# Optimization experiments

Measured on AMD Instinct MI355X. Metric: run time of the kernel, lower is better.

## Reference

```python
import jax, jax.numpy as jnp
import numpy as np

B, S, D, UNITS = 8, 2048, 1024, 1024

def setup_inputs() -> dict:
    key = jax.random.key(0)
    k1, k2, k3, k4 = jax.random.split(key, 4)
    scale = 1.0 / np.sqrt(D)
    return {
        "inputs": jax.random.normal(k1, (B, S, D), dtype=jnp.float32),
        "Wq": jax.random.normal(k2, (D, UNITS), dtype=jnp.float32) * scale,
        "Wk": jax.random.normal(k3, (D, UNITS), dtype=jnp.float32) * scale,
        "Wv": jax.random.normal(k4, (D, UNITS), dtype=jnp.float32) * scale,
    }

def reference(inputs, Wq, Wk, Wv):
    # QKV projections (bias-free Dense): [B,S,D] @ [D,U] -> [B,S,U]
    q = jnp.einsum("bsd,du->bsu", inputs, Wq)
    k = jnp.einsum("bsd,du->bsu", inputs, Wk)
    v = jnp.einsum("bsd,du->bsu", inputs, Wv)
    # scaled dot-product scores [B,S,S]
    scores = jnp.einsum("bqu,bku->bqk", q, k) / jnp.sqrt(jnp.float32(UNITS))
    attn = jax.nn.softmax(scores, axis=-1)
    # weighted sum of values [B,S,U]
    return jnp.einsum("bqk,bku->bqu", attn, v)
```

## Files before the change

kernel.cpp:

```cpp
#include <hip/hip_runtime.h>


typedef _Float16 half8  __attribute__((ext_vector_type(8)));
typedef _Float16 half4v __attribute__((ext_vector_type(4)));
typedef _Float16 half2v __attribute__((ext_vector_type(2)));
typedef float    floatx4 __attribute__((ext_vector_type(4)));

__device__ __forceinline__ void stage_ht(const _Float16* __restrict__ src, int ld,
                                         _Float16* __restrict__ dst, int wave, int lane) {
#pragma unroll
    for (int i = 0; i < 2; ++i) {
        int q = wave * 2 + i;
        int c = q * 64 + lane;
        int row = c >> 3, c8 = c & 7;
        int cg = c8 ^ (row & 7);
        __builtin_amdgcn_global_load_lds(
            (const __attribute__((address_space(1))) unsigned int*)(src + (size_t)row * ld + cg * 8),
            (__attribute__((address_space(3))) unsigned int*)(dst + q * 512),
            16, 0, 0);
    }
}

__device__ __forceinline__ float sum8h(half8 a) {
    union { half8 v; half2v h2[4]; } u; u.v = a;
    half2v s0 = u.h2[0] + u.h2[1];
    half2v s1 = u.h2[2] + u.h2[3];
    half2v s  = s0 + s1;
    return (float)s[0] + (float)s[1];
}

#define BARF() do { __builtin_amdgcn_s_barrier(); asm volatile("" ::: "memory"); } while (0)

#define SA_(T, h) stage_ht(A + (size_t)((h) * 128) * lda + (size_t)(T) * 64, lda, \
                           ShA + (((T) & 1) * 2 + (h)) * 8192, wave, lane)
#define SB_(T, h) stage_ht(B + (size_t)((h) * 128) * ldb + (size_t)(T) * 64, ldb, \
                           ShB + (((T) & 1) * 2 + (h)) * 8192, wave, lane)

__device__ __forceinline__ void read_b(const _Float16* __restrict__ Bs, int rb,
                                       int l15, int q4, int kk, half8 (&bf)[4]) {
#pragma unroll
    for (int j = 0; j < 4; ++j) {
        int rr = rb + j * 16 + l15;
        int cg = (kk * 4 + q4) ^ (rr & 7);
        bf[j] = *(const half8*)(Bs + rr * 64 + cg * 8);
    }
}

template<bool RSUM>
__device__ __forceinline__ void read_a(const _Float16* __restrict__ As, int i0,
                                       int l15, int q4, int kk, half8 (&af)[4],
                                       float* rsum) {
#pragma unroll
    for (int ii = 0; ii < 4; ++ii) {
        int rr = (i0 + ii) * 16 + l15;
        int cg = (kk * 4 + q4) ^ (rr & 7);
        af[ii] = *(const half8*)(As + rr * 64 + cg * 8);
        if (RSUM) rsum[i0 + ii] += sum8h(af[ii]);
    }
}

__device__ __forceinline__ void mfma16(const half8 (&af)[4], const half8 (&bf)[4],
                                       int i0, floatx4 (&acc)[8][4]) {
    asm volatile("s_waitcnt lgkmcnt(0)" ::: "memory");
    __builtin_amdgcn_sched_barrier(0);
    __builtin_amdgcn_s_setprio(1);
#pragma unroll
    for (int ii = 0; ii < 4; ++ii)
#pragma unroll
        for (int j = 0; j < 4; ++j)
            acc[i0 + ii][j] = __builtin_amdgcn_mfma_f32_16x16x32_f16(
                af[ii], bf[j], acc[i0 + ii][j], 0, 0, 0);
    __builtin_amdgcn_s_setprio(0);
}

template<bool RSUM>
__device__ __forceinline__ void gemm8p(const _Float16* __restrict__ A, int lda,
                                       const _Float16* __restrict__ B, int ldb,
                                       int K, _Float16* __restrict__ ShA,
                                       _Float16* __restrict__ ShB,
                                       int wave, int lane,
                                       floatx4 (&acc)[8][4], float (&rsum)[8]) {
    const int wm = wave >> 2, wn = wave & 3;
    const int l15 = lane & 15, q4 = lane >> 4;
    const int NT = K >> 6;

    SB_(0, 0); SB_(0, 1); SA_(0, 0); SA_(0, 1);
    SB_(1, 0); SB_(1, 1);
    asm volatile("s_waitcnt vmcnt(4)" ::: "memory");
    BARF();

    for (int t = 0; t < NT; ++t) {
        const _Float16* As = ShA + (t & 1) * 16384 + wm * 8192;
        const _Float16* Bs = ShB + (t & 1) * 16384 + (wn >> 1) * 8192;
        const int rb = (wn & 1) * 64;
        half8 bf[4], af[4];

        read_b(Bs, rb, l15, q4, 0, bf);
        read_a<RSUM>(As, 0, l15, q4, 0, af, rsum);
        if (t + 1 < NT) SA_(t + 1, 0);
        BARF();
        mfma16(af, bf, 0, acc);
        BARF();

        read_a<RSUM>(As, 4, l15, q4, 0, af, rsum);
        if (t + 1 < NT) SA_(t + 1, 1);
        BARF();
        mfma16(af, bf, 4, acc);
        BARF();

        read_b(Bs, rb, l15, q4, 1, bf);
        read_a<RSUM>(As, 0, l15, q4, 1, af, rsum);
        BARF();
        mfma16(af, bf, 0, acc);
        BARF();

        read_a<RSUM>(As, 4, l15, q4, 1, af, rsum);
        if (t + 2 < NT) { SB_(t + 2, 0); SB_(t + 2, 1); }
        BARF();
        mfma16(af, bf, 4, acc);
        if (t + 1 < NT) {
            if (t + 2 < NT) asm volatile("s_waitcnt vmcnt(4)" ::: "memory");
            else            asm volatile("s_waitcnt vmcnt(0)" ::: "memory");
        }
        BARF();
    }
}

__global__ void cast_x(const float* __restrict__ X, _Float16* __restrict__ Xh) {
    size_t i = ((size_t)blockIdx.x * 256 + threadIdx.x) * 8;
    float4 v0 = *(const float4*)(X + i);
    float4 v1 = *(const float4*)(X + i + 4);
    half8 hh;
    hh[0] = (_Float16)v0.x; hh[1] = (_Float16)v0.y; hh[2] = (_Float16)v0.z; hh[3] = (_Float16)v0.w;
    hh[4] = (_Float16)v1.x; hh[5] = (_Float16)v1.y; hh[6] = (_Float16)v1.z; hh[7] = (_Float16)v1.w;
    *(half8*)(Xh + i) = hh;
}

__global__ void prep_weights(const float* __restrict__ Wq, const float* __restrict__ Wk,
                             const float* __restrict__ Wv, _Float16* __restrict__ WbT) {
    int g = blockIdx.z;
    const float* W = (g == 0) ? Wq : (g == 1) ? Wk : Wv;
    __shared__ float tile[32][33];
    int u0 = blockIdx.x * 32, d0 = blockIdx.y * 32;
    int tx = threadIdx.x & 31, ty = threadIdx.x >> 5;
#pragma unroll
    for (int i = 0; i < 32; i += 8)
        tile[ty + i][tx] = W[(size_t)(d0 + ty + i) * 1024 + (u0 + tx)];
    __syncthreads();
#pragma unroll
    for (int i = 0; i < 32; i += 8)
        WbT[(size_t)g * 1024 * 1024 + (size_t)(u0 + ty + i) * 1024 + (d0 + tx)] =
            (_Float16)tile[tx][ty + i];
}

__global__ __launch_bounds__(512, 2)
void qkv_gemm(const _Float16* __restrict__ Xh, const _Float16* __restrict__ WbT,
              _Float16* __restrict__ Qh, _Float16* __restrict__ Kh,
              _Float16* __restrict__ Vt) {
    __shared__ __align__(16) _Float16 ShA[32768];
    __shared__ __align__(16) _Float16 ShB[32768];
    int t = threadIdx.x;
    int lane = t & 63, wave = t >> 6;
    int wm = wave >> 2, wn = wave & 3;
    int l15 = lane & 15, q4 = lane >> 4;
    int which = blockIdx.x >> 2;
    int u0 = (blockIdx.x & 3) * 256;
    int m0 = blockIdx.y * 256;
    const _Float16* A = Xh + (size_t)m0 * 1024;
    const _Float16* B = WbT + (size_t)which * 1024 * 1024 + (size_t)u0 * 1024;
    floatx4 acc[8][4] = {};
    float rsum[8] = {};
    gemm8p<false>(A, 1024, B, 1024, 1024, ShA, ShB, wave, lane, acc, rsum);

    int bz = m0 >> 11;
    int sbase = (m0 & 2047) + wm * 128;
    if (which < 2) {
        _Float16* db = (which ? Kh : Qh) + (size_t)bz * 2048 * 1024;
#pragma unroll
        for (int i = 0; i < 8; ++i)
#pragma unroll
            for (int j = 0; j < 4; ++j)
#pragma unroll
                for (int r = 0; r < 4; ++r) {
                    int s = sbase + i * 16 + q4 * 4 + r;
                    int u = u0 + wn * 64 + j * 16 + l15;
                    db[(size_t)s * 1024 + u] = (_Float16)acc[i][j][r];
                }
    } else {
        _Float16* vb = Vt + (size_t)bz * 1024 * 2048;
#pragma unroll
        for (int i = 0; i < 8; ++i)
#pragma unroll
            for (int j = 0; j < 4; ++j) {
                int s = sbase + i * 16 + q4 * 4;
                int u = u0 + wn * 64 + j * 16 + l15;
                half4v pk;
#pragma unroll
                for (int r = 0; r < 4; ++r) pk[r] = (_Float16)acc[i][j][r];
                *(half4v*)(vb + (size_t)u * 2048 + s) = pk;
            }
    }
}

__global__ __launch_bounds__(512, 2)
void scores_gemm(const _Float16* __restrict__ Qh, const _Float16* __restrict__ Kh,
                 _Float16* __restrict__ P) {
    __shared__ __align__(16) _Float16 ShA[32768];
    __shared__ __align__(16) _Float16 ShB[32768];
    int t = threadIdx.x;
    int lane = t & 63, wave = t >> 6;
    int wm = wave >> 2, wn = wave & 3;
    int l15 = lane & 15, q4 = lane >> 4;
    int m0 = blockIdx.y * 256, n0 = blockIdx.x * 256;
    int batch = blockIdx.z;
    const _Float16* A = Qh + (size_t)batch * 2048 * 1024 + (size_t)m0 * 1024;
    const _Float16* B = Kh + (size_t)batch * 2048 * 1024 + (size_t)n0 * 1024;
    floatx4 acc[8][4] = {};
    float rsum[8] = {};
    gemm8p<false>(A, 1024, B, 1024, 1024, ShA, ShB, wave, lane, acc, rsum);

    _Float16* Pb = P + (size_t)batch * 2048 * 2048;
#pragma unroll
    for (int i = 0; i < 8; ++i)
#pragma unroll
        for (int j = 0; j < 4; ++j)
#pragma unroll
            for (int r = 0; r < 4; ++r) {
                int m = m0 + wm * 128 + i * 16 + q4 * 4 + r;
                int n = n0 + wn * 64 + j * 16 + l15;
                Pb[(size_t)m * 2048 + n] = (_Float16)__expf(acc[i][j][r] * 0.03125f);
            }
}

__global__ __launch_bounds__(512, 2)
void pv_gemm(const _Float16* __restrict__ P, const _Float16* __restrict__ Vt,
             float* __restrict__ out) {
    __shared__ __align__(16) _Float16 ShA[32768];
    __shared__ __align__(16) _Float16 ShB[32768];
    int t = threadIdx.x;
    int lane = t & 63, wave = t >> 6;
    int wm = wave >> 2, wn = wave & 3;
    int l15 = lane & 15, q4 = lane >> 4;
    int m0 = blockIdx.y * 256, n0 = blockIdx.x * 256;
    int batch = blockIdx.z;
    const _Float16* A = P + (size_t)batch * 2048 * 2048 + (size_t)m0 * 2048;
    const _Float16* B = Vt + (size_t)batch * 1024 * 2048 + (size_t)n0 * 2048;
    floatx4 acc[8][4] = {};
    float rsum[8] = {};
    gemm8p<true>(A, 2048, B, 2048, 2048, ShA, ShB, wave, lane, acc, rsum);

    float rsumf[8];
#pragma unroll
    for (int i = 0; i < 8; ++i) {
        float v = rsum[i] + __shfl_xor(rsum[i], 16);
        rsumf[i] = v + __shfl_xor(v, 32);
    }
    float* ob = out + (size_t)batch * 2048 * 1024;
#pragma unroll
    for (int i = 0; i < 8; ++i)
#pragma unroll
        for (int r = 0; r < 4; ++r) {
            int rloc = q4 * 4 + r;
            float inv = 1.0f / __shfl(rsumf[i], rloc);
            int m = m0 + wm * 128 + i * 16 + rloc;
#pragma unroll
            for (int j = 0; j < 4; ++j) {
                int n = n0 + wn * 64 + j * 16 + l15;
                ob[(size_t)m * 1024 + n] = acc[i][j][r] * inv;
            }
        }
}

extern "C" void kernel_launch(void* const* d_in, const int* in_sizes, int n_in,
                              void* d_out, int out_size, void* d_ws, size_t ws_size,
                              hipStream_t stream) {
    const float* X  = (const float*)d_in[0];
    const float* Wq = (const float*)d_in[1];
    const float* Wk = (const float*)d_in[2];
    const float* Wv = (const float*)d_in[3];
    float* out = (float*)d_out;

    char* ws = (char*)d_ws;
    size_t off = 0;
    _Float16* Xh  = (_Float16*)(ws + off); off += (size_t)8 * 2048 * 1024 * 2;
    _Float16* WbT = (_Float16*)(ws + off); off += (size_t)3 * 1024 * 1024 * 2;
    _Float16* Qh  = (_Float16*)(ws + off); off += (size_t)8 * 2048 * 1024 * 2;
    _Float16* Kh  = (_Float16*)(ws + off); off += (size_t)8 * 2048 * 1024 * 2;
    _Float16* Vt  = (_Float16*)(ws + off); off += (size_t)8 * 1024 * 2048 * 2;
    _Float16* P   = (_Float16*)(ws + off); off += (size_t)8 * 2048 * 2048 * 2;

    cast_x      <<<dim3(8192, 1, 1), 256, 0, stream>>>(X, Xh);
    prep_weights<<<dim3(32, 32, 3), 256, 0, stream>>>(Wq, Wk, Wv, WbT);
    qkv_gemm    <<<dim3(12, 64, 1), 512, 0, stream>>>(Xh, WbT, Qh, Kh, Vt);
    scores_gemm <<<dim3(8, 8, 8),   512, 0, stream>>>(Qh, Kh, P);
    pv_gemm     <<<dim3(4, 8, 8),   512, 0, stream>>>(P, Vt, out);
}
```

Measured before the change: 390.4 us.

## Replace ping-pong barrier schedule with simple double-buffered prefetch per K tile

Removes the fine-grained read/MFMA phases split by four barriers per K tile, and the explicit waitcnt, sched_barrier and setprio hints. Each iteration now issues global-to-LDS loads for the whole next tile, runs a fused LDS-read plus MFMA loop, then waits on all loads and takes one barrier. This cuts barrier overhead and gives the compiler freedom to interleave LDS reads with MFMAs. In exchange it loses the deeper B-tile prefetch and the explicit wave-interleaving control, so load latency may be less well hidden.

New measurement: 419.1 us. +7.4%, slower.

```diff
diff --git a/kernel.cpp b/kernel.cpp
--- a/kernel.cpp
+++ b/kernel.cpp
@@ -36,41 +36,32 @@
 #define SB_(T, h) stage_ht(B + (size_t)((h) * 128) * ldb + (size_t)(T) * 64, ldb, \
                            ShB + (((T) & 1) * 2 + (h)) * 8192, wave, lane)
 
-__device__ __forceinline__ void read_b(const _Float16* __restrict__ Bs, int rb,
-                                       int l15, int q4, int kk, half8 (&bf)[4]) {
-#pragma unroll
-    for (int j = 0; j < 4; ++j) {
-        int rr = rb + j * 16 + l15;
-        int cg = (kk * 4 + q4) ^ (rr & 7);
-        bf[j] = *(const half8*)(Bs + rr * 64 + cg * 8);
-    }
-}
-
 template<bool RSUM>
-__device__ __forceinline__ void read_a(const _Float16* __restrict__ As, int i0,
-                                       int l15, int q4, int kk, half8 (&af)[4],
-                                       float* rsum) {
-#pragma unroll
-    for (int ii = 0; ii < 4; ++ii) {
-        int rr = (i0 + ii) * 16 + l15;
-        int cg = (kk * 4 + q4) ^ (rr & 7);
-        af[ii] = *(const half8*)(As + rr * 64 + cg * 8);
-        if (RSUM) rsum[i0 + ii] += sum8h(af[ii]);
-    }
-}
-
-__device__ __forceinline__ void mfma16(const half8 (&af)[4], const half8 (&bf)[4],
-                                       int i0, floatx4 (&acc)[8][4]) {
-    asm volatile("s_waitcnt lgkmcnt(0)" ::: "memory");
-    __builtin_amdgcn_sched_barrier(0);
-    __builtin_amdgcn_s_setprio(1);
-#pragma unroll
-    for (int ii = 0; ii < 4; ++ii)
-#pragma unroll
-        for (int j = 0; j < 4; ++j)
-            acc[i0 + ii][j] = __builtin_amdgcn_mfma_f32_16x16x32_f16(
-                af[ii], bf[j], acc[i0 + ii][j], 0, 0, 0);
-    __builtin_amdgcn_s_setprio(0);
+__device__ __forceinline__ void tile_body(const _Float16* __restrict__ As,
+                                          const _Float16* __restrict__ Bs,
+                                          int rb, int l15, int q4,
+                                          floatx4 (&acc)[8][4], float (&rsum)[8]) {
+#pragma unroll
+    for (int kk = 0; kk < 2; ++kk) {
+        half8 bf[4];
+#pragma unroll
+        for (int j = 0; j < 4; ++j) {
+            int rr = rb + j * 16 + l15;
+            int cg = (kk * 4 + q4) ^ (rr & 7);
+            bf[j] = *(const half8*)(Bs + rr * 64 + cg * 8);
+        }
+#pragma unroll
+        for (int i = 0; i < 8; ++i) {
+            int rr = i * 16 + l15;
+            int cg = (kk * 4 + q4) ^ (rr & 7);
+            half8 af = *(const half8*)(As + rr * 64 + cg * 8);
+            if (RSUM) rsum[i] += sum8h(af);
+#pragma unroll
+            for (int j = 0; j < 4; ++j)
+                acc[i][j] = __builtin_amdgcn_mfma_f32_16x16x32_f16(
+                    af, bf[j], acc[i][j], 0, 0, 0);
+        }
+    }
 }
 
 template<bool RSUM>
@@ -85,44 +76,21 @@
     const int NT = K >> 6;
 
     SB_(0, 0); SB_(0, 1); SA_(0, 0); SA_(0, 1);
-    SB_(1, 0); SB_(1, 1);
-    asm volatile("s_waitcnt vmcnt(4)" ::: "memory");
+    asm volatile("s_waitcnt vmcnt(0)" ::: "memory");
     BARF();
 
     for (int t = 0; t < NT; ++t) {
         const _Float16* As = ShA + (t & 1) * 16384 + wm * 8192;
         const _Float16* Bs = ShB + (t & 1) * 16384 + (wn >> 1) * 8192;
-        const int rb = (wn & 1) * 64;
-        half8 bf[4], af[4];
-
-        read_b(Bs, rb, l15, q4, 0, bf);
-        read_a<RSUM>(As, 0, l15, q4, 0, af, rsum);
-        if (t + 1 < NT) SA_(t + 1, 0);
-        BARF();
-        mfma16(af, bf, 0, acc);
-        BARF();
-
-        read_a<RSUM>(As, 4, l15, q4, 0, af, rsum);
-        if (t + 1 < NT) SA_(t + 1, 1);
-        BARF();
-        mfma16(af, bf, 4, acc);
-        BARF();
-
-        read_b(Bs, rb, l15, q4, 1, bf);
-        read_a<RSUM>(As, 0, l15, q4, 1, af, rsum);
-        BARF();
-        mfma16(af, bf, 0, acc);
-        BARF();
-
-        read_a<RSUM>(As, 4, l15, q4, 1, af, rsum);
-        if (t + 2 < NT) { SB_(t + 2, 0); SB_(t + 2, 1); }
-        BARF();
-        mfma16(af, bf, 4, acc);
+
+        if (t + 1 < NT) { SA_(t + 1, 0); SA_(t + 1, 1); SB_(t + 1, 0); SB_(t + 1, 1); }
+
+        tile_body<RSUM>(As, Bs, (wn & 1) * 64, l15, q4, acc, rsum);
+
         if (t + 1 < NT) {
-            if (t + 2 < NT) asm volatile("s_waitcnt vmcnt(4)" ::: "memory");
-            else            asm volatile("s_waitcnt vmcnt(0)" ::: "memory");
-        }
-        BARF();
+            asm volatile("s_waitcnt vmcnt(0)" ::: "memory");
+            BARF();
+        }
     }
 }
 
```

## Replace pipelined QKV GEMM with simple 128x128 tile single-buffered kernel

Applied to the files above, without the earlier changes.

The QKV projection kernel drops the shared double-buffered 256x256 pipelined GEMM in favor of a simpler 128x128 tile kernel with 256 threads, single-buffered LDS staging and two barriers per K step. This raises grid size and occupancy, with smaller LDS and register use per block. In exchange it loses load/compute overlap and halves data reuse per tile, which increases global and L2 traffic.

Measured after the change: 399.4 us. 1.02x slower.

```diff
diff --git a/kernel.cpp b/kernel.cpp
--- a/kernel.cpp
+++ b/kernel.cpp
@@ -5,6 +5,61 @@
 typedef _Float16 half4v __attribute__((ext_vector_type(4)));
 typedef _Float16 half2v __attribute__((ext_vector_type(2)));
 typedef float    floatx4 __attribute__((ext_vector_type(4)));
+
+
+__device__ __forceinline__ float sum8h(half8 a) {
+    union { half8 v; half2v h2[4]; } u; u.v = a;
+    half2v s0 = u.h2[0] + u.h2[1];
+    half2v s1 = u.h2[2] + u.h2[3];
+    half2v s  = s0 + s1;
+    return (float)s[0] + (float)s[1];
+}
+
+#define BARF() do { __builtin_amdgcn_s_barrier(); asm volatile("" ::: "memory"); } while (0)
+
+
+__device__ __forceinline__ void stage_async4(const _Float16* __restrict__ src, int ld,
+                                             _Float16* __restrict__ dst, int wave, int lane) {
+#pragma unroll
+    for (int i = 0; i < 4; ++i) {
+        int chunk = i * 4 + wave;
+        int L = chunk * 64 + lane;
+        int row = L >> 3, c8 = L & 7;
+        int cg = c8 ^ (row & 7);
+        __builtin_amdgcn_global_load_lds(
+            (const __attribute__((address_space(1))) unsigned int*)(src + (size_t)row * ld + cg * 8),
+            (__attribute__((address_space(3))) unsigned int*)(dst + chunk * 512),
+            16, 0, 0);
+    }
+}
+
+__device__ __forceinline__ void mfma_accum44(const _Float16* __restrict__ As,
+                                             const _Float16* __restrict__ Bs,
+                                             int wm, int wn, int l15, int q4,
+                                             floatx4 acc[4][4]) {
+#pragma unroll
+    for (int kk = 0; kk < 2; ++kk) {
+        half8 a[4], b[4];
+#pragma unroll
+        for (int i = 0; i < 4; ++i) {
+            int row = wm * 64 + i * 16 + l15;
+            int cg = (kk * 4 + q4) ^ (row & 7);
+            a[i] = *(const half8*)(As + row * 64 + cg * 8);
+        }
+#pragma unroll
+        for (int j = 0; j < 4; ++j) {
+            int row = wn * 64 + j * 16 + l15;
+            int cg = (kk * 4 + q4) ^ (row & 7);
+            b[j] = *(const half8*)(Bs + row * 64 + cg * 8);
+        }
+#pragma unroll
+        for (int i = 0; i < 4; ++i)
+#pragma unroll
+            for (int j = 0; j < 4; ++j)
+                acc[i][j] = __builtin_amdgcn_mfma_f32_16x16x32_f16(a[i], b[j], acc[i][j], 0, 0, 0);
+    }
+}
+
 
 __device__ __forceinline__ void stage_ht(const _Float16* __restrict__ src, int ld,
                                          _Float16* __restrict__ dst, int wave, int lane) {
@@ -20,16 +75,6 @@
             16, 0, 0);
     }
 }
-
-__device__ __forceinline__ float sum8h(half8 a) {
-    union { half8 v; half2v h2[4]; } u; u.v = a;
-    half2v s0 = u.h2[0] + u.h2[1];
-    half2v s1 = u.h2[2] + u.h2[3];
-    half2v s  = s0 + s1;
-    return (float)s[0] + (float)s[1];
-}
-
-#define BARF() do { __builtin_amdgcn_s_barrier(); asm volatile("" ::: "memory"); } while (0)
 
 #define SA_(T, h) stage_ht(A + (size_t)((h) * 128) * lda + (size_t)(T) * 64, lda, \
                            ShA + (((T) & 1) * 2 + (h)) * 8192, wave, lane)
@@ -126,6 +171,7 @@
     }
 }
 
+
 __global__ void cast_x(const float* __restrict__ X, _Float16* __restrict__ Xh) {
     size_t i = ((size_t)blockIdx.x * 256 + threadIdx.x) * 8;
     float4 v0 = *(const float4*)(X + i);
@@ -153,31 +199,33 @@
             (_Float16)tile[tx][ty + i];
 }
 
-__global__ __launch_bounds__(512, 2)
-void qkv_gemm(const _Float16* __restrict__ Xh, const _Float16* __restrict__ WbT,
-              _Float16* __restrict__ Qh, _Float16* __restrict__ Kh,
-              _Float16* __restrict__ Vt) {
-    __shared__ __align__(16) _Float16 ShA[32768];
-    __shared__ __align__(16) _Float16 ShB[32768];
+__global__ void qkv_gemm(const _Float16* __restrict__ Xh, const _Float16* __restrict__ WbT,
+                         _Float16* __restrict__ Qh, _Float16* __restrict__ Kh,
+                         _Float16* __restrict__ Vt) {
+    __shared__ __align__(16) _Float16 As[128 * 64];
+    __shared__ __align__(16) _Float16 Bs[128 * 64];
     int t = threadIdx.x;
     int lane = t & 63, wave = t >> 6;
-    int wm = wave >> 2, wn = wave & 3;
+    int wm = wave >> 1, wn = wave & 1;
     int l15 = lane & 15, q4 = lane >> 4;
-    int which = blockIdx.x >> 2;
-    int u0 = (blockIdx.x & 3) * 256;
-    int m0 = blockIdx.y * 256;
-    const _Float16* A = Xh + (size_t)m0 * 1024;
-    const _Float16* B = WbT + (size_t)which * 1024 * 1024 + (size_t)u0 * 1024;
-    floatx4 acc[8][4] = {};
-    float rsum[8] = {};
-    gemm8p<false>(A, 1024, B, 1024, 1024, ShA, ShB, wave, lane, acc, rsum);
-
-    int bz = m0 >> 11;
-    int sbase = (m0 & 2047) + wm * 128;
+    int m0 = blockIdx.y * 128, n0 = blockIdx.x * 128;
+    floatx4 acc[4][4] = {};
+    for (int kt = 0; kt < 1024; kt += 64) {
+        __syncthreads();
+        stage_async4(Xh + (size_t)m0 * 1024 + kt, 1024, As, wave, lane);
+        stage_async4(WbT + (size_t)n0 * 1024 + kt, 1024, Bs, wave, lane);
+        __syncthreads();
+        mfma_accum44(As, Bs, wm, wn, l15, q4, acc);
+    }
+    int which = blockIdx.x >> 3;
+    int u0 = (blockIdx.x & 7) * 128;
+    int b = m0 >> 11;
+    int sbase = (m0 & 2047) + wm * 64;
     if (which < 2) {
-        _Float16* db = (which ? Kh : Qh) + (size_t)bz * 2048 * 1024;
-#pragma unroll
-        for (int i = 0; i < 8; ++i)
+        _Float16* dst = which ? Kh : Qh;
+        _Float16* db = dst + (size_t)b * 2048 * 1024;
+#pragma unroll
+        for (int i = 0; i < 4; ++i)
 #pragma unroll
             for (int j = 0; j < 4; ++j)
 #pragma unroll
@@ -187,9 +235,9 @@
                     db[(size_t)s * 1024 + u] = (_Float16)acc[i][j][r];
                 }
     } else {
-        _Float16* vb = Vt + (size_t)bz * 1024 * 2048;
-#pragma unroll
-        for (int i = 0; i < 8; ++i)
+        _Float16* vb = Vt + (size_t)b * 1024 * 2048;
+#pragma unroll
+        for (int i = 0; i < 4; ++i)
 #pragma unroll
             for (int j = 0; j < 4; ++j) {
                 int s = sbase + i * 16 + q4 * 4;
@@ -291,7 +339,7 @@
 
     cast_x      <<<dim3(8192, 1, 1), 256, 0, stream>>>(X, Xh);
     prep_weights<<<dim3(32, 32, 3), 256, 0, stream>>>(Wq, Wk, Wv, WbT);
-    qkv_gemm    <<<dim3(12, 64, 1), 512, 0, stream>>>(Xh, WbT, Qh, Kh, Vt);
+    qkv_gemm    <<<dim3(24, 128, 1), 256, 0, stream>>>(Xh, WbT, Qh, Kh, Vt);
     scores_gemm <<<dim3(8, 8, 8),   512, 0, stream>>>(Qh, Kh, P);
     pv_gemm     <<<dim3(4, 8, 8),   512, 0, stream>>>(P, Vt, out);
 }
```
